# Kernel tuning notes

Hardware: AMD Instinct MI355X
Metric: run time of the kernel (lower is better)

## Reference

```python
import jax, jax.numpy as jnp
import numpy as np

B, TQ, TK = 2, 1024, 2048
DQ, DC, H, TOPK = 1024, 768, 16, 64
DH = DQ // H


def setup_inputs() -> dict:
    key = jax.random.key(0)
    ks = jax.random.split(key, 12)
    s = lambda d: 1.0 / np.sqrt(d)
    return {
        "x": jax.random.normal(ks[0], (B, TQ, DQ), jnp.float32),
        "context": jax.random.normal(ks[1], (B, TK, DC), jnp.float32),
        "key_padding_mask": jax.random.bernoulli(ks[2], 0.05, (B, TK)),
        "Wq": jax.random.normal(ks[3], (DQ, DQ), jnp.float32) * s(DQ),
        "bq": jnp.zeros((DQ,), jnp.float32),
        "Wk": jax.random.normal(ks[4], (DC, DQ), jnp.float32) * s(DC),
        "bk": jnp.zeros((DQ,), jnp.float32),
        "Wv": jax.random.normal(ks[5], (DC, DQ), jnp.float32) * s(DC),
        "bv": jnp.zeros((DQ,), jnp.float32),
        "Wo": jax.random.normal(ks[6], (DQ, DQ), jnp.float32) * s(DQ),
        "bo": jnp.zeros((DQ,), jnp.float32),
    }


def _heads(t):
    # (B, T, DQ) -> (B, H, T, DH)
    b, tt, _ = t.shape
    return t.reshape(b, tt, H, DH).transpose(0, 2, 1, 3)


def reference(x, context, key_padding_mask, Wq, bq, Wk, bk, Wv, bv, Wo, bo):
    q = _heads(x @ Wq + bq)          # (B,H,Tq,DH)
    k = _heads(context @ Wk + bk)    # (B,H,Tk,DH)
    v = _heads(context @ Wv + bv)    # (B,H,Tk,DH)

    scale = DH ** -0.5
    logits = jnp.einsum("bhqd,bhkd->bhqk", q, k) * scale  # (B,H,Tq,Tk)
    neg = jnp.finfo(logits.dtype).min
    logits = jnp.where(key_padding_mask[:, None, None, :], neg, logits)

    # hard top-k sparsification: keep top TOPK logits per query, fill rest with -inf-like
    topk_vals, topk_idx = jax.lax.top_k(logits, TOPK)
    sparse_logits = jnp.full_like(logits, neg)
    sparse_logits = jnp.put_along_axis(sparse_logits, topk_idx, topk_vals, axis=-1, inplace=False)

    attn = jax.nn.softmax(sparse_logits, axis=-1)
    out = jnp.einsum("bhqk,bhkd->bhqd", attn, v)  # (B,H,Tq,DH)
    out = out.transpose(0, 2, 1, 3).reshape(B, TQ, DQ)
    return out @ Wo + bo
```

## Files before the change

### kernel.cpp

```cpp
#include <hip/hip_runtime.h>
#include <cstdint>
#include <cstddef>

#define BN_ 2
#define TQ_ 1024
#define TK_ 2048
#define DQ_ 1024
#define DC_ 768
#define NH_ 16
#define DH_ 64
#define TOPK_ 64

typedef unsigned short u16;
typedef __attribute__((ext_vector_type(8))) short short8;
typedef __attribute__((ext_vector_type(8))) u16   ushort8;
typedef __attribute__((ext_vector_type(4))) float floatx4;

__device__ __forceinline__ float bf2f(u16 u) { return __uint_as_float(((unsigned)u) << 16); }
__device__ __forceinline__ u16 f2bf(float f) {
    unsigned u = __float_as_uint(f);
    u += 0x7FFFu + ((u >> 16) & 1u);
    return (u16)(u >> 16);
}
__device__ __forceinline__ float definite(float v, float repl) {
    return ((__float_as_uint(v) & 0x7F800000u) == 0x7F800000u) ? repl : v;
}
__device__ __forceinline__ unsigned mono(float f) {
    unsigned u = __float_as_uint(f);
    return (u & 0x80000000u) ? ~u : (u | 0x80000000u);
}
__device__ __forceinline__ float invmono(unsigned u) {
    return __uint_as_float((u & 0x80000000u) ? (u & 0x7FFFFFFFu) : ~u);
}
__device__ __forceinline__ void gld16(const u16* g, u16* l) {
    __builtin_amdgcn_global_load_lds(
        (const __attribute__((address_space(1))) unsigned*)g,
        (__attribute__((address_space(3))) unsigned*)l, 16, 0, 0);
}
__device__ __forceinline__ int gsum16(int x) {
#pragma unroll
    for (int o = 1; o < 16; o <<= 1) x += __shfl_xor(x, o);
    return x;
}
__device__ __forceinline__ int gmin16(int x) {
#pragma unroll
    for (int o = 1; o < 16; o <<= 1) { int y = __shfl_xor(x, o); x = (y < x) ? y : x; }
    return x;
}
__device__ __forceinline__ unsigned gmin16u(unsigned x) {
#pragma unroll
    for (int o = 1; o < 16; o <<= 1) { unsigned y = __shfl_xor((int)x, o); x = (y < x) ? y : x; }
    return x;
}
__device__ __forceinline__ unsigned gmax16u(unsigned x) {
#pragma unroll
    for (int o = 1; o < 16; o <<= 1) { unsigned y = __shfl_xor((int)x, o); x = (y > x) ? y : x; }
    return x;
}
__device__ __forceinline__ float gmax16f(float x) {
#pragma unroll
    for (int o = 1; o < 16; o <<= 1) x = fmaxf(x, __shfl_xor(x, o));
    return x;
}
__device__ __forceinline__ float gsum16f(float x) {
#pragma unroll
    for (int o = 1; o < 16; o <<= 1) x += __shfl_xor(x, o);
    return x;
}

__global__ void marker_kernel(float* __restrict__ out, int n, float val) {
    const int i = blockIdx.x * 256 + threadIdx.x;
    if (i < n) out[i] = val;
}

__device__ __forceinline__ float select_topk32_ik(const unsigned (&um)[32], int l16,
                                                  float* cvrow, int* ckrow) {
    unsigned X = 0u;
    bool done = false;
    for (int bit = 31; bit >= 0; --bit) {
        const unsigned C = X | (1u << bit);
        int c = 0;
#pragma unroll
        for (int j = 0; j < 32; ++j) c += (um[j] >= C) ? 1 : 0;
        c = gsum16(c);
        if (!done && c >= 64) X = C;
        if (c == 64) done = true;
        if (__all(done)) break;
    }
    int myGt = 0;
#pragma unroll
    for (int j = 0; j < 32; ++j) myGt += (um[j] > X) ? 1 : 0;
    const int totalGt = gsum16(myGt);
    int pre = myGt;
#pragma unroll
    for (int off = 1; off < 16; off <<= 1) {
        const int tv = __shfl_up(pre, off);
        if (l16 >= off) pre += tv;
    }
    int wpos = pre - myGt;
#pragma unroll
    for (int j = 0; j < 32; ++j) {
        if (um[j] > X) {
            cvrow[wpos] = invmono(um[j]);
            ckrow[wpos] = (l16 + 16 * j) << 11;
            ++wpos;
        }
    }
    const float xval = invmono(X);
    int remaining = 64 - totalGt;
    int pos = totalGt;
    int lastkey = -1;
    while (remaining > 0) {
        int mykey = 0x7FFFFFFF;
#pragma unroll
        for (int j = 0; j < 32; ++j) {
            const int kj = (l16 + 16 * j) << 11;
            if (um[j] == X && kj > lastkey && kj < mykey) mykey = kj;
        }
        const int mn = gmin16(mykey);
        if (mn == 0x7FFFFFFF) break;
        if (mykey == mn) { cvrow[pos] = xval; ckrow[pos] = mn; }
        lastkey = mn;
        ++pos; --remaining;
    }
    return xval;
}

template <int NV>
__device__ __forceinline__ float select_topk(const unsigned (&um)[NV], const int (&kk)[NV],
                                             unsigned base, int hb, int l16,
                                             float* cvrow, int* ckrow) {
    unsigned X = 0u;
    bool done = false;
    for (int bit = hb; bit >= 0; --bit) {
        const unsigned C = X | (1u << bit);
        int c = 0;
#pragma unroll
        for (int j = 0; j < NV; ++j) c += (um[j] >= C) ? 1 : 0;
        c = gsum16(c);
        if (!done && c >= 64) X = C;
        if (c == 64) done = true;
        if (__all(done)) break;
    }
    int myGt = 0;
#pragma unroll
    for (int j = 0; j < NV; ++j) myGt += (um[j] > X) ? 1 : 0;
    const int totalGt = gsum16(myGt);
    int pre = myGt;
#pragma unroll
    for (int off = 1; off < 16; off <<= 1) {
        const int tv = __shfl_up(pre, off);
        if (l16 >= off) pre += tv;
    }
    int wpos = pre - myGt;
#pragma unroll
    for (int j = 0; j < NV; ++j) {
        if (um[j] > X) {
            cvrow[wpos] = invmono(base + um[j]);
            ckrow[wpos] = kk[j];
            ++wpos;
        }
    }
    const float xval = invmono(base + X);
    int remaining = 64 - totalGt;
    int pos = totalGt;
    int lastkey = -1;
    while (remaining > 0) {
        int mykey = 0x7FFFFFFF;
#pragma unroll
        for (int j = 0; j < NV; ++j)
            if (um[j] == X && kk[j] > lastkey && kk[j] < mykey) mykey = kk[j];
        const int mn = gmin16(mykey);
        if (mn == 0x7FFFFFFF) break;
        if (mykey == mn) { cvrow[pos] = xval; ckrow[pos] = mn; }
        lastkey = mn;
        ++pos; --remaining;
    }
    return xval;
}

struct TsplitJob { const float* W; u16* Wh; u16* Wl; int K; int N; };

__global__ void __launch_bounds__(256) tsplit3(TsplitJob j0, TsplitJob j1, TsplitJob j2) {
    const TsplitJob j = (blockIdx.z == 0) ? j0 : (blockIdx.z == 1) ? j1 : j2;
    const int bk = blockIdx.y * 32;
    if (bk >= j.K) return;
    __shared__ float t[32][33];
    const int x = threadIdx.x & 31, y = threadIdx.x >> 5;
    const int bn = blockIdx.x * 32;
#pragma unroll
    for (int i = 0; i < 32; i += 8) t[y + i][x] = j.W[(size_t)(bk + y + i) * j.N + bn + x];
    __syncthreads();
#pragma unroll
    for (int i = 0; i < 32; i += 8) {
        const float f = t[x][y + i];
        const u16 hi = f2bf(f);
        const size_t o = (size_t)(bn + y + i) * j.K + bk + x;
        j.Wh[o] = hi;
        j.Wl[o] = f2bf(f - bf2f(hi));
    }
}

__global__ void __launch_bounds__(256) tsplit(const float* __restrict__ W,
                                              u16* __restrict__ Wh, u16* __restrict__ Wl,
                                              int K, int N) {
    __shared__ float t[32][33];
    const int x = threadIdx.x & 31, y = threadIdx.x >> 5;
    const int bn = blockIdx.x * 32, bk = blockIdx.y * 32;
#pragma unroll
    for (int i = 0; i < 32; i += 8) t[y + i][x] = W[(size_t)(bk + y + i) * N + bn + x];
    __syncthreads();
#pragma unroll
    for (int i = 0; i < 32; i += 8) {
        const float f = t[x][y + i];
        const u16 hi = f2bf(f);
        const size_t o = (size_t)(bn + y + i) * K + bk + x;
        Wh[o] = hi;
        Wl[o] = f2bf(f - bf2f(hi));
    }
}

template <int ASPLIT, int OMODE>
__global__ void __launch_bounds__(256) gemm3(
    const void* __restrict__ Ap, const void* __restrict__ Alp,
    const u16* __restrict__ Bh, const u16* __restrict__ Bl,
    const float* __restrict__ bias, float scale,
    void* __restrict__ out0, void* __restrict__ out1,
    int M, int N, int K) {
    __shared__ u16 Ahs[64 * 64];
    __shared__ u16 Als[64 * 64];
    __shared__ u16 Bhs[128 * 64];
    __shared__ u16 Bls[128 * 64];

    const int tid = threadIdx.x;
    const int lane = tid & 63, wave = tid >> 6;
    const int wm = wave >> 1, wn = wave & 1;
    const int quad = lane >> 4, l16 = lane & 15;
    const int bm = blockIdx.y * 64, bn = blockIdx.x * 128;

    floatx4 acc[2][4] = {};

    for (int k0 = 0; k0 < K; k0 += 64) {
        __syncthreads();
#pragma unroll
        for (int s2 = 0; s2 < 2; ++s2) {
            const int slot = tid + s2 * 256;
            const int m = slot >> 3, cpos = slot & 7;
            const int c = cpos ^ (m & 7);
            const size_t aoff = (size_t)(bm + m) * K + k0 + c * 8;
            if constexpr (ASPLIT == 0) {
                const float* f = (const float*)Ap + aoff;
                const floatx4 a = *(const floatx4*)f;
                const floatx4 b = *(const floatx4*)(f + 4);
                ushort8 hi, lo;
#pragma unroll
                for (int j = 0; j < 4; ++j) {
                    u16 t = f2bf(a[j]);
                    hi[j] = t; lo[j] = f2bf(a[j] - bf2f(t));
                    t = f2bf(b[j]);
                    hi[4 + j] = t; lo[4 + j] = f2bf(b[j] - bf2f(t));
                }
                *(ushort8*)&Ahs[slot * 8] = hi;
                *(ushort8*)&Als[slot * 8] = lo;
            } else {
                gld16((const u16*)Ap  + aoff, &Ahs[slot * 8]);
                gld16((const u16*)Alp + aoff, &Als[slot * 8]);
            }
        }
#pragma unroll
        for (int s4 = 0; s4 < 4; ++s4) {
            const int slot = tid + s4 * 256;
            const int n = slot >> 3, cpos = slot & 7;
            const int c = cpos ^ (n & 7);
            const size_t boff = (size_t)(bn + n) * K + k0 + c * 8;
            gld16(Bh + boff, &Bhs[slot * 8]);
            gld16(Bl + boff, &Bls[slot * 8]);
        }
        __syncthreads();
#pragma unroll
        for (int s = 0; s < 2; ++s) {
            short8 ah[2], al[2], bh[4], bl[4];
#pragma unroll
            for (int mt = 0; mt < 2; ++mt) {
                const int m = wm * 32 + mt * 16 + l16;
                const int cs = s * 4 + quad;
                const int slot = m * 8 + (cs ^ (m & 7));
                ah[mt] = *(const short8*)&Ahs[slot * 8];
                al[mt] = *(const short8*)&Als[slot * 8];
            }
#pragma unroll
            for (int nt = 0; nt < 4; ++nt) {
                const int n = wn * 64 + nt * 16 + l16;
                const int cs = s * 4 + quad;
                const int slot = n * 8 + (cs ^ (n & 7));
                bh[nt] = *(const short8*)&Bhs[slot * 8];
                bl[nt] = *(const short8*)&Bls[slot * 8];
            }
#pragma unroll
            for (int mt = 0; mt < 2; ++mt)
#pragma unroll
                for (int nt = 0; nt < 4; ++nt) {
                    acc[mt][nt] = __builtin_amdgcn_mfma_f32_16x16x32_bf16(ah[mt], bh[nt], acc[mt][nt], 0, 0, 0);
                    acc[mt][nt] = __builtin_amdgcn_mfma_f32_16x16x32_bf16(al[mt], bh[nt], acc[mt][nt], 0, 0, 0);
                    acc[mt][nt] = __builtin_amdgcn_mfma_f32_16x16x32_bf16(ah[mt], bl[nt], acc[mt][nt], 0, 0, 0);
                }
        }
    }

#pragma unroll
    for (int mt = 0; mt < 2; ++mt) {
#pragma unroll
        for (int nt = 0; nt < 4; ++nt) {
            const int col = bn + wn * 64 + nt * 16 + l16;
            const float bcol = bias[col];
#pragma unroll
            for (int r = 0; r < 4; ++r) {
                const int row = bm + wm * 32 + mt * 16 + quad * 4 + r;
                const float val = definite((acc[mt][nt][r] + bcol) * scale, 0.0f);
                const size_t idx = (size_t)row * N + col;
                if constexpr (OMODE == 0) {
                    ((float*)out0)[idx] = val;
                } else if constexpr (OMODE == 1) {
                    ((u16*)out0)[idx] = f2bf(val);
                } else {
                    const u16 hi = f2bf(val);
                    ((u16*)out0)[idx] = hi;
                    ((u16*)out1)[idx] = f2bf(val - bf2f(hi));
                }
            }
        }
    }
}

struct GemmKVJob { const u16* Bh; const u16* Bl; const float* bias;
                   void* out0; void* out1; int omode; };

__global__ void __launch_bounds__(256) gemm_kv(
    const float* __restrict__ Ap, GemmKVJob j0, GemmKVJob j1,
    int M, int N, int K) {
    const GemmKVJob j = (blockIdx.z == 0) ? j0 : j1;
    __shared__ u16 Ahs[64 * 64];
    __shared__ u16 Als[64 * 64];
    __shared__ u16 Bhs[128 * 64];
    __shared__ u16 Bls[128 * 64];

    const int tid = threadIdx.x;
    const int lane = tid & 63, wave = tid >> 6;
    const int wm = wave >> 1, wn = wave & 1;
    const int quad = lane >> 4, l16 = lane & 15;
    const int bm = blockIdx.y * 64, bn = blockIdx.x * 128;

    floatx4 acc[2][4] = {};

    for (int k0 = 0; k0 < K; k0 += 64) {
        __syncthreads();
#pragma unroll
        for (int s2 = 0; s2 < 2; ++s2) {
            const int slot = tid + s2 * 256;
            const int m = slot >> 3, cpos = slot & 7;
            const int c = cpos ^ (m & 7);
            const size_t aoff = (size_t)(bm + m) * K + k0 + c * 8;
            const float* f = Ap + aoff;
            const floatx4 a = *(const floatx4*)f;
            const floatx4 b = *(const floatx4*)(f + 4);
            ushort8 hi, lo;
#pragma unroll
            for (int jj = 0; jj < 4; ++jj) {
                u16 t = f2bf(a[jj]);
                hi[jj] = t; lo[jj] = f2bf(a[jj] - bf2f(t));
                t = f2bf(b[jj]);
                hi[4 + jj] = t; lo[4 + jj] = f2bf(b[jj] - bf2f(t));
            }
            *(ushort8*)&Ahs[slot * 8] = hi;
            *(ushort8*)&Als[slot * 8] = lo;
        }
#pragma unroll
        for (int s4 = 0; s4 < 4; ++s4) {
            const int slot = tid + s4 * 256;
            const int n = slot >> 3, cpos = slot & 7;
            const int c = cpos ^ (n & 7);
            const size_t boff = (size_t)(bn + n) * K + k0 + c * 8;
            gld16(j.Bh + boff, &Bhs[slot * 8]);
            gld16(j.Bl + boff, &Bls[slot * 8]);
        }
        __syncthreads();
#pragma unroll
        for (int s = 0; s < 2; ++s) {
            short8 ah[2], al[2], bh[4], bl[4];
#pragma unroll
            for (int mt = 0; mt < 2; ++mt) {
                const int m = wm * 32 + mt * 16 + l16;
                const int cs = s * 4 + quad;
                const int slot = m * 8 + (cs ^ (m & 7));
                ah[mt] = *(const short8*)&Ahs[slot * 8];
                al[mt] = *(const short8*)&Als[slot * 8];
            }
#pragma unroll
            for (int nt = 0; nt < 4; ++nt) {
                const int n = wn * 64 + nt * 16 + l16;
                const int cs = s * 4 + quad;
                const int slot = n * 8 + (cs ^ (n & 7));
                bh[nt] = *(const short8*)&Bhs[slot * 8];
                bl[nt] = *(const short8*)&Bls[slot * 8];
            }
#pragma unroll
            for (int mt = 0; mt < 2; ++mt)
#pragma unroll
                for (int nt = 0; nt < 4; ++nt) {
                    acc[mt][nt] = __builtin_amdgcn_mfma_f32_16x16x32_bf16(ah[mt], bh[nt], acc[mt][nt], 0, 0, 0);
                    acc[mt][nt] = __builtin_amdgcn_mfma_f32_16x16x32_bf16(al[mt], bh[nt], acc[mt][nt], 0, 0, 0);
                    acc[mt][nt] = __builtin_amdgcn_mfma_f32_16x16x32_bf16(ah[mt], bl[nt], acc[mt][nt], 0, 0, 0);
                }
        }
    }

#pragma unroll
    for (int mt = 0; mt < 2; ++mt) {
#pragma unroll
        for (int nt = 0; nt < 4; ++nt) {
            const int col = bn + wn * 64 + nt * 16 + l16;
            const float bcol = j.bias[col];
#pragma unroll
            for (int r = 0; r < 4; ++r) {
                const int row = bm + wm * 32 + mt * 16 + quad * 4 + r;
                const float val = definite(acc[mt][nt][r] + bcol, 0.0f);
                const size_t idx = (size_t)row * N + col;
                if (j.omode == 1) {
                    ((u16*)j.out0)[idx] = f2bf(val);
                } else {
                    const u16 hi = f2bf(val);
                    ((u16*)j.out0)[idx] = hi;
                    ((u16*)j.out1)[idx] = f2bf(val - bf2f(hi));
                }
            }
        }
    }
}

__global__ void __launch_bounds__(256, 4) attn_topk(
    const u16* Qhi, const u16* Qlo,
    const u16* __restrict__ Khi, const u16* __restrict__ Klo,
    const u16* __restrict__ Vb16, const void* __restrict__ maskp,
    u16* attnH, u16* attnL) {
    __shared__ float lg[16][512];

#define CV_(row) (&lg[row][256])
#define CK_(row) (((int*)&lg[row][0]) + 320)

    const int tid = threadIdx.x;
    const int lane = tid & 63, wave = tid >> 6;
    const int quad = lane >> 4, l16 = lane & 15;
    const int rowg = wave * 4 + quad;
    const int b = blockIdx.z, h = blockIdx.y, q0 = blockIdx.x * 16;

    int mmode;
    {
        bool cbyte = false, cbf = false, cf32 = false;
#pragma unroll
        for (int j = 0; j < 16; ++j) {
            const int i = lane + 64 * j;
            const unsigned v = ((const u16*)maskp)[i];
            cbyte |= (v == 0x0100u || v == 0x0101u) || ((i & 1) && v == 0x0001u);
            cbf   |= (!(i & 1)) && v == 0x3F80u;
            cf32  |= (i & 1) && v == 0x3F80u;
        }
        const bool abf = __any(cbf), af32 = __any(cf32), abyte = __any(cbyte);
        mmode = abf ? 2 : (af32 ? 3 : (abyte ? 1 : 0));
    }

    short8 qh[2], ql[2];
    {
        const size_t base = (size_t)(b * TQ_ + q0 + l16) * DQ_ + h * DH_ + quad * 8;
        qh[0] = *(const short8*)(Qhi + base);
        qh[1] = *(const short8*)(Qhi + base + 32);
        ql[0] = *(const short8*)(Qlo + base);
        ql[1] = *(const short8*)(Qlo + base + 32);
    }

    for (int qtr = 0; qtr < 4; ++qtr) {
        if (qtr == 0) {
#pragma unroll 2
            for (int t = 0; t < 8; ++t) {
                const int key = wave * 128 + t * 16 + l16;
                const size_t kb = (size_t)(b * TK_ + key) * DQ_ + h * DH_ + quad * 8;
                const short8 kh0 = *(const short8*)(Khi + kb);
                const short8 kh1 = *(const short8*)(Khi + kb + 32);
                const short8 kl0 = *(const short8*)(Klo + kb);
                const short8 kl1 = *(const short8*)(Klo + kb + 32);
                floatx4 acc = {};
                acc = __builtin_amdgcn_mfma_f32_16x16x32_bf16(qh[0], kh0, acc, 0, 0, 0);
                acc = __builtin_amdgcn_mfma_f32_16x16x32_bf16(ql[0], kh0, acc, 0, 0, 0);
                acc = __builtin_amdgcn_mfma_f32_16x16x32_bf16(qh[0], kl0, acc, 0, 0, 0);
                acc = __builtin_amdgcn_mfma_f32_16x16x32_bf16(qh[1], kh1, acc, 0, 0, 0);
                acc = __builtin_amdgcn_mfma_f32_16x16x32_bf16(ql[1], kh1, acc, 0, 0, 0);
                acc = __builtin_amdgcn_mfma_f32_16x16x32_bf16(qh[1], kl1, acc, 0, 0, 0);
                const int midx = b * TK_ + key;
                bool masked;
                if (mmode == 2)      masked = ((const u16*)maskp)[midx] != 0;
                else if (mmode == 3) masked = ((const float*)maskp)[midx] != 0.0f;
                else if (mmode == 1) masked = ((const unsigned char*)maskp)[midx] != 0;
                else                 masked = ((const int*)maskp)[midx] != 0;
#pragma unroll
                for (int r = 0; r < 4; ++r)
                    lg[quad * 4 + r][key] = masked ? -3.0e38f : acc[r];
            }
            __syncthreads();

            unsigned um[32];
#pragma unroll
            for (int j = 0; j < 32; ++j) um[j] = mono(lg[rowg][l16 + 16 * j]);
            const float th = select_topk32_ik(um, l16, CV_(rowg), CK_(rowg));
            if (l16 == 0) {
                lg[rowg][255] = th;
                ((int*)&lg[rowg][0])[511] = 0;
            }
        } else {
            float cmrow[4];
#pragma unroll
            for (int r = 0; r < 4; ++r) cmrow[r] = lg[quad * 4 + r][255];
#pragma unroll 2
            for (int t = 0; t < 8; ++t) {
                const int key = qtr * 512 + wave * 128 + t * 16 + l16;
                const size_t kb = (size_t)(b * TK_ + key) * DQ_ + h * DH_ + quad * 8;
                const short8 kh0 = *(const short8*)(Khi + kb);
                const short8 kh1 = *(const short8*)(Khi + kb + 32);
                const short8 kl0 = *(const short8*)(Klo + kb);
                const short8 kl1 = *(const short8*)(Klo + kb + 32);
                floatx4 acc = {};
                acc = __builtin_amdgcn_mfma_f32_16x16x32_bf16(qh[0], kh0, acc, 0, 0, 0);
                acc = __builtin_amdgcn_mfma_f32_16x16x32_bf16(ql[0], kh0, acc, 0, 0, 0);
                acc = __builtin_amdgcn_mfma_f32_16x16x32_bf16(qh[0], kl0, acc, 0, 0, 0);
                acc = __builtin_amdgcn_mfma_f32_16x16x32_bf16(qh[1], kh1, acc, 0, 0, 0);
                acc = __builtin_amdgcn_mfma_f32_16x16x32_bf16(ql[1], kh1, acc, 0, 0, 0);
                acc = __builtin_amdgcn_mfma_f32_16x16x32_bf16(qh[1], kl1, acc, 0, 0, 0);
                const int midx = b * TK_ + key;
                bool masked;
                if (mmode == 2)      masked = ((const u16*)maskp)[midx] != 0;
                else if (mmode == 3) masked = ((const float*)maskp)[midx] != 0.0f;
                else if (mmode == 1) masked = ((const unsigned char*)maskp)[midx] != 0;
                else                 masked = ((const int*)maskp)[midx] != 0;
#pragma unroll
                for (int r = 0; r < 4; ++r) {
                    const float val = masked ? -3.0e38f : acc[r];
                    if (val > cmrow[r]) {
                        const int row = quad * 4 + r;
                        const int pos = atomicAdd((int*)&lg[row][511], 1);
                        if (pos < 127) {
                            lg[row][pos] = val;
                            ((int*)&lg[row][0])[128 + pos] = key << 11;
                        }
                    }
                }
            }
            __syncthreads();

            unsigned uc[4]; int ck4[4];
#pragma unroll
            for (int t = 0; t < 4; ++t) {
                uc[t] = mono(CV_(rowg)[l16 + 16 * t]);
                ck4[t] = CK_(rowg)[l16 + 16 * t];
            }
            unsigned cm = uc[0];
            cm = (uc[1] < cm) ? uc[1] : cm;
            cm = (uc[2] < cm) ? uc[2] : cm;
            cm = (uc[3] < cm) ? uc[3] : cm;
            cm = gmin16u(cm);
            int cnt = ((int*)&lg[rowg][0])[511];
            if (cnt > 127) cnt = 127;

            unsigned zm[12]; int kk[12];
            unsigned zmx = 0;
#pragma unroll
            for (int i = 0; i < 8; ++i) {
                const int idx = l16 + 16 * i;
                const bool valid = idx < cnt;
                const float v = lg[rowg][idx];
                const int k = ((int*)&lg[rowg][0])[128 + idx];
                const unsigned mv = mono(v);
                const bool live = valid && (mv > cm);
                zm[i] = live ? (mv - cm) : 0u;
                kk[i] = live ? k : 0x7FFFFFFF;
                zmx = (zm[i] > zmx) ? zm[i] : zmx;
            }
#pragma unroll
            for (int t = 0; t < 4; ++t) {
                zm[8 + t] = uc[t] - cm;
                kk[8 + t] = ck4[t];
                zmx = (zm[8 + t] > zmx) ? zm[8 + t] : zmx;
            }
            zmx = gmax16u(zmx);
            const int hb = 31 - __clz(zmx | 1u);
            const float th = select_topk<12>(zm, kk, cm, hb, l16, CV_(rowg), CK_(rowg));
            if (l16 == 0) {
                lg[rowg][255] = th;
                ((int*)&lg[rowg][0])[511] = 0;
            }
        }
        if (qtr < 3) __syncthreads();
    }

    {
        float v4[4];
#pragma unroll
        for (int t = 0; t < 4; ++t) v4[t] = CV_(rowg)[l16 + 16 * t];
        float m = fmaxf(fmaxf(v4[0], v4[1]), fmaxf(v4[2], v4[3]));
        m = gmax16f(m);
        float p4[4], S = 0.f;
#pragma unroll
        for (int t = 0; t < 4; ++t) { p4[t] = __expf(v4[t] - m); S += p4[t]; }
        S = gsum16f(S);
        const float inv = 1.0f / S;
#pragma unroll
        for (int t = 0; t < 4; ++t) CV_(rowg)[l16 + 16 * t] = p4[t] * inv;
    }

    const int half = lane >> 5, l32 = lane & 31;
    const char* Vrow = (const char*)(Vb16 + (size_t)b * TK_ * DQ_ + h * DH_ + l32 * 2);
#pragma unroll
    for (int rp = 0; rp < 2; ++rp) {
        const int row = wave * 4 + rp * 2 + half;
        float a0 = 0.f, a1 = 0.f;
#pragma unroll 4
        for (int e = 0; e < 64; ++e) {
            const float w = CV_(row)[e];
            const int koff = CK_(row)[e];
            const unsigned v2 = *(const unsigned*)(Vrow + koff);
            a0 = fmaf(w, __uint_as_float(v2 << 16), a0);
            a1 = fmaf(w, __uint_as_float(v2 & 0xFFFF0000u), a1);
        }
        a0 = definite(a0, 0.0f);
        a1 = definite(a1, 0.0f);
        const size_t o = (size_t)(b * TQ_ + q0 + row) * DQ_ + h * DH_ + l32 * 2;
        const u16 h0 = f2bf(a0), h1 = f2bf(a1);
        const u16 l0 = f2bf(a0 - bf2f(h0)), l1 = f2bf(a1 - bf2f(h1));
        *(unsigned*)(attnH + o) = (unsigned)h0 | ((unsigned)h1 << 16);
        *(unsigned*)(attnL + o) = (unsigned)l0 | ((unsigned)l1 << 16);
    }
#undef CV_
#undef CK_
}

extern "C" void kernel_launch(void* const* d_in, const int* in_sizes, int n_in,
                              void* d_out, int out_size, void* d_ws, size_t ws_size,
                              hipStream_t stream) {
    static const int exp_sizes[11] = {2097152, 3145728, 4096, 1048576, 1024,
                                      786432, 1024, 786432, 1024, 1048576, 1024};
    if (n_in != 11) {
        marker_kernel<<<(out_size + 255) / 256, 256, 0, stream>>>((float*)d_out, out_size,
                                                                  (float)(150 + n_in));
        return;
    }
    for (int i = 0; i < 11; ++i)
        if (in_sizes[i] != exp_sizes[i]) {
            marker_kernel<<<(out_size + 255) / 256, 256, 0, stream>>>((float*)d_out, out_size,
                                                                      (float)(200 + i));
            return;
        }

    const float* x   = (const float*)d_in[0];
    const float* ctx = (const float*)d_in[1];
    const void*  msk = d_in[2];
    const float* Wq = (const float*)d_in[3];
    const float* bq = (const float*)d_in[4];
    const float* Wk = (const float*)d_in[5];
    const float* bk = (const float*)d_in[6];
    const float* Wv = (const float*)d_in[7];
    const float* bv = (const float*)d_in[8];
    const float* Wo = (const float*)d_in[9];
    const float* bo = (const float*)d_in[10];

    const size_t SZ_Q = (size_t)BN_ * TQ_ * DQ_ * 2;
    const size_t SZ_K = (size_t)BN_ * TK_ * DQ_ * 2;
    const size_t NEED = 2 * SZ_Q + 2 * SZ_K + SZ_K;
    if (ws_size < NEED) {
        marker_kernel<<<(out_size + 255) / 256, 256, 0, stream>>>(
            (float*)d_out, out_size, (float)(ws_size >> 20));
        return;
    }

    char* ws = (char*)d_ws;
    u16* Qhi = (u16*)(ws);
    u16* Qlo = (u16*)(ws + SZ_Q);
    u16* Khi = (u16*)(ws + 2 * SZ_Q);
    u16* Klo = (u16*)(ws + 2 * SZ_Q + SZ_K);
    u16* Vb  = (u16*)(ws + 2 * SZ_Q + 2 * SZ_K);

    u16* WqT_h = Khi;
    u16* WqT_l = Khi + (size_t)DQ_ * DQ_;
    u16* WvT_h = (u16*)d_out;
    u16* WvT_l = WvT_h + (size_t)DC_ * DQ_;
    u16* WkT_h = WvT_h + 2 * (size_t)DC_ * DQ_;
    u16* WkT_l = WvT_h + 3 * (size_t)DC_ * DQ_;
    u16* WoT_h = Khi;
    u16* WoT_l = Khi + (size_t)DQ_ * DQ_;

    const int MQ = BN_ * TQ_;
    const int MK = BN_ * TK_;

    TsplitJob jq{Wq, WqT_h, WqT_l, DQ_, DQ_};
    TsplitJob jk{Wk, WkT_h, WkT_l, DC_, DQ_};
    TsplitJob jv{Wv, WvT_h, WvT_l, DC_, DQ_};
    tsplit3<<<dim3(DQ_ / 32, DQ_ / 32, 3), 256, 0, stream>>>(jq, jk, jv);

    gemm3<0, 2><<<dim3(DQ_ / 128, MQ / 64), 256, 0, stream>>>(
        x, nullptr, WqT_h, WqT_l, bq, 0.125f, Qhi, Qlo, MQ, DQ_, DQ_);

    GemmKVJob jobK{WkT_h, WkT_l, bk, Khi, Klo, 2};
    GemmKVJob jobV{WvT_h, WvT_l, bv, Vb, nullptr, 1};
    gemm_kv<<<dim3(DQ_ / 128, MK / 64, 2), 256, 0, stream>>>(
        ctx, jobK, jobV, MK, DQ_, DC_);

    attn_topk<<<dim3(TQ_ / 16, NH_, BN_), 256, 0, stream>>>(
        Qhi, Qlo, Khi, Klo, Vb, msk, Qhi, Qlo);

    tsplit<<<dim3(DQ_ / 32, DQ_ / 32), 256, 0, stream>>>(Wo, WoT_h, WoT_l, DQ_, DQ_);
    gemm3<1, 0><<<dim3(DQ_ / 128, MQ / 64), 256, 0, stream>>>(
        Qhi, Qlo, WoT_h, WoT_l, bo, 1.0f, d_out, nullptr, MQ, DQ_, DQ_);
}
```

Before: 410.6 us.

## Swizzle logits LDS layout, remap attention block order, use bf16 conversion intrinsic

Three separate changes. The hand-written float-to-bf16 rounding in the GEMM A-tile split becomes the HIP __float2bfloat16 intrinsic, which may map to a hardware convert instruction. The attention kernel's block index is permuted so consecutive blocks are spread across (batch, head, query) tiles, likely to balance work across XCDs and improve cache locality. Writes and reads of the per-row logits in LDS now XOR the column with a row-dependent swizzle to reduce bank conflicts. The swizzle is only shown in the first pass, so any other reads of lg rows in unseen code would have to match it.

Result: slower. 447.0 us (+8.9%).

```diff
diff --git a/kernel.cpp b/kernel.cpp
--- a/kernel.cpp
+++ b/kernel.cpp
@@ -1,4 +1,5 @@
 #include <hip/hip_runtime.h>
+#include <hip/hip_bf16.h>
 #include <cstdint>
 #include <cstddef>
 
@@ -22,6 +23,11 @@
     u += 0x7FFFu + ((u >> 16) & 1u);
     return (u16)(u >> 16);
 }
+__device__ __forceinline__ u16 f2bf_cvt(float f) {
+    union { __hip_bfloat16 b; u16 u; } cv;
+    cv.b = __float2bfloat16(f);
+    return cv.u;
+}
 __device__ __forceinline__ float definite(float v, float repl) {
     return ((__float_as_uint(v) & 0x7F800000u) == 0x7F800000u) ? repl : v;
 }
@@ -66,6 +72,9 @@
 #pragma unroll
     for (int o = 1; o < 16; o <<= 1) x += __shfl_xor(x, o);
     return x;
+}
+__device__ __forceinline__ int lgswz(int row) {
+    return ((((row >> 2) ^ row) & 1) << 4) | (((row >> 1) & 1) << 2);
 }
 
 __global__ void marker_kernel(float* __restrict__ out, int n, float val) {
@@ -255,10 +264,10 @@
                 ushort8 hi, lo;
 #pragma unroll
                 for (int j = 0; j < 4; ++j) {
-                    u16 t = f2bf(a[j]);
-                    hi[j] = t; lo[j] = f2bf(a[j] - bf2f(t));
-                    t = f2bf(b[j]);
-                    hi[4 + j] = t; lo[4 + j] = f2bf(b[j] - bf2f(t));
+                    const u16 t = f2bf_cvt(a[j]);
+                    hi[j] = t; lo[j] = f2bf_cvt(a[j] - bf2f(t));
+                    const u16 t2 = f2bf_cvt(b[j]);
+                    hi[4 + j] = t2; lo[4 + j] = f2bf_cvt(b[j] - bf2f(t2));
                 }
                 *(ushort8*)&Ahs[slot * 8] = hi;
                 *(ushort8*)&Als[slot * 8] = lo;
@@ -366,10 +375,10 @@
             ushort8 hi, lo;
 #pragma unroll
             for (int jj = 0; jj < 4; ++jj) {
-                u16 t = f2bf(a[jj]);
-                hi[jj] = t; lo[jj] = f2bf(a[jj] - bf2f(t));
-                t = f2bf(b[jj]);
-                hi[4 + jj] = t; lo[4 + jj] = f2bf(b[jj] - bf2f(t));
+                const u16 t = f2bf_cvt(a[jj]);
+                hi[jj] = t; lo[jj] = f2bf_cvt(a[jj] - bf2f(t));
+                const u16 t2 = f2bf_cvt(b[jj]);
+                hi[4 + jj] = t2; lo[4 + jj] = f2bf_cvt(b[jj] - bf2f(t2));
             }
             *(ushort8*)&Ahs[slot * 8] = hi;
             *(ushort8*)&Als[slot * 8] = lo;
@@ -451,7 +460,10 @@
     const int lane = tid & 63, wave = tid >> 6;
     const int quad = lane >> 4, l16 = lane & 15;
     const int rowg = wave * 4 + quad;
-    const int b = blockIdx.z, h = blockIdx.y, q0 = blockIdx.x * 16;
+    const int flat = blockIdx.x + 64 * (blockIdx.y + 16 * blockIdx.z);
+    const int swzb = (flat & 7) * 256 + (flat >> 3);
+    const int b = swzb >> 10, h = (swzb >> 6) & 15, q0 = (swzb & 63) * 16;
+    const int sRow = lgswz(rowg);
 
     int mmode;
     {
@@ -501,14 +513,17 @@
                 else if (mmode == 1) masked = ((const unsigned char*)maskp)[midx] != 0;
                 else                 masked = ((const int*)maskp)[midx] != 0;
 #pragma unroll
-                for (int r = 0; r < 4; ++r)
-                    lg[quad * 4 + r][key] = masked ? -3.0e38f : acc[r];
+                for (int r = 0; r < 4; ++r) {
+                    const int row = quad * 4 + r;
+                    lg[row][key ^ lgswz(row)] = masked ? -3.0e38f : acc[r];
+                }
             }
             __syncthreads();
 
             unsigned um[32];
 #pragma unroll
-            for (int j = 0; j < 32; ++j) um[j] = mono(lg[rowg][l16 + 16 * j]);
+            for (int j = 0; j < 32; ++j)
+                um[j] = mono(lg[rowg][(l16 + 16 * j) ^ sRow]);
             const float th = select_topk32_ik(um, l16, CV_(rowg), CK_(rowg));
             if (l16 == 0) {
                 lg[rowg][255] = th;
```
